# Performance work log

Measured on AMD Instinct MI355X. Metric: run time of the kernel, lower is better.

Reference implementation:

```python
import jax, jax.numpy as jnp
import numpy as np

N_NODES = 100000
N_EDGES = 3200000
F_IN = 128
F_HID = 16
F_OUT = 1


def setup_inputs() -> dict:
    key = jax.random.key(0)
    ks = jax.random.split(key, 8)
    x = jax.random.normal(ks[0], (N_NODES, F_IN), dtype=jnp.float32)
    src = jax.random.randint(ks[1], (N_EDGES,), 0, N_NODES, dtype=jnp.int32)
    dst = jax.random.randint(ks[2], (N_EDGES,), 0, N_NODES, dtype=jnp.int32)
    edge_w = jax.random.uniform(ks[3], (N_EDGES,), dtype=jnp.float32)
    W0 = jax.random.normal(ks[4], (F_IN, F_HID), dtype=jnp.float32) / np.sqrt(F_IN)
    b0 = jnp.zeros((F_HID,), dtype=jnp.float32)
    W1 = jax.random.normal(ks[5], (F_HID, F_OUT), dtype=jnp.float32) / np.sqrt(F_HID)
    b1 = jnp.zeros((F_OUT,), dtype=jnp.float32)
    return {"x": x, "src": src, "dst": dst, "edge_w": edge_w,
            "W0": W0, "b0": b0, "W1": W1, "b1": b1}


def _spmm(src, dst, edge_w, h):
    # sparse A (COO) @ dense h: gather rows at src, weight, scatter-add to dst
    msgs = h[src] * edge_w[:, None]            # [E, F]
    return jax.ops.segment_sum(msgs, dst, num_segments=N_NODES)  # [N, F]


def reference(x, src, dst, edge_w, W0, b0, W1, b1):
    # GCNConv layer 0: relu(A @ (x @ W0) + b0)
    z0 = x @ W0                                 # [N, 16] linear transform first
    h = jax.nn.relu(_spmm(src, dst, edge_w, z0) + b0)
    # (Dropout is identity at inference)
    # GCNConv layer 1: sigmoid(A @ (h @ W1) + b1)
    z1 = h @ W1                                 # [N, 1]
    out = jax.nn.sigmoid(_spmm(src, dst, edge_w, z1) + b1)
    return out
```

## Files before the change

### kernel.cpp

```cpp
#include <hip/hip_runtime.h>

#define N_NODES 100000
#define N_EDGES 3200000
#define F_IN 128
#define F_HID 16

#define BK_LG 7
#define BK_NODES 128
#define NB ((N_NODES + BK_NODES - 1) / BK_NODES)
#define BCAPF 4736
#define CLG 10
#define CNODES 1024
#define NBC ((N_NODES + CNODES - 1) / CNODES)
#define NBC_P 128
#define BCAPC 34816
#define CHUNK1 2048
#define NCH1 ((N_EDGES + CHUNK1 - 1) / CHUNK1)
#define CHUNKM 2048
#define CPB2 ((BCAPC + CHUNKM - 1) / CHUNKM)
#define NMB (NBC * CPB2)
#define NXB ((N_NODES + 63) / 64)
#define PAIRED (2 * NXB)
#define GRID_MID (NMB + NXB)
#define CUR_STRIDE 16

__device__ __forceinline__ unsigned short f2bf_rne(float f) {
    unsigned u = __float_as_uint(f);
    u += 0x7FFFu + ((u >> 16) & 1u);
    return (unsigned short)(u >> 16);
}

__global__ __launch_bounds__(256) void k_bin1(const int* __restrict__ src,
                                              const int* __restrict__ dst,
                                              const float* __restrict__ ew,
                                              int* __restrict__ cursorC,
                                              int2* __restrict__ ebinC) {
    __shared__ int2 stage[CHUNK1];
    __shared__ unsigned char sbid[CHUNK1];
    __shared__ int cnt[NBC_P], excl[NBC_P], run[NBC_P], gb[NBC_P], alw[NBC_P];
    __shared__ int wtot[2];
    const int tid = threadIdx.x;
    const int e0  = blockIdx.x * CHUNK1;
    const int nch = min(CHUNK1, N_EDGES - e0);

    for (int i = tid; i < NBC_P; i += 256) cnt[i] = 0;
    __syncthreads();

    int es[8], eb[8], edl[8]; float ww[8];
    #pragma unroll
    for (int k = 0; k < 8; ++k) {
        int idx = k * 256 + tid;
        if (idx < nch) {
            int e = e0 + idx;
            int d = dst[e];
            es[k]  = src[e];
            ww[k]  = ew[e];
            eb[k]  = d >> CLG;
            edl[k] = d & (CNODES - 1);
            atomicAdd(&cnt[eb[k]], 1);
        } else {
            eb[k] = -1;
        }
    }
    __syncthreads();

    {
        const int lane = tid & 63;
        int inc = 0, dv_ = 0;
        if (tid < NBC_P) {
            dv_ = cnt[tid];
            inc = dv_;
            #pragma unroll
            for (int off = 1; off < 64; off <<= 1) {
                int t = __shfl_up(inc, off);
                if (lane >= off) inc += t;
            }
            if (lane == 63) wtot[tid >> 6] = inc;
        }
        __syncthreads();
        if (tid < NBC_P) {
            int base = (tid >= 64) ? wtot[0] : 0;
            excl[tid] = base + inc - dv_;
        }
    }
    __syncthreads();

    if (tid < NBC) {
        int c = cnt[tid];
        if (c > 0) {
            int old = atomicAdd(&cursorC[tid * CUR_STRIDE], c);
            int a = BCAPC - old;
            a = (a < 0) ? 0 : ((a > c) ? c : a);
            alw[tid] = a;
            gb[tid]  = tid * BCAPC + old;
        } else {
            alw[tid] = 0;
            gb[tid]  = tid * BCAPC;
        }
        run[tid] = 0;
    }
    __syncthreads();

    #pragma unroll
    for (int k = 0; k < 8; ++k) {
        if (eb[k] >= 0) {
            int b = eb[k];
            int p = excl[b] + atomicAdd(&run[b], 1);
            stage[p] = make_int2(__float_as_int(ww[k]), es[k] | (edl[k] << 17));
            sbid[p]  = (unsigned char)b;
        }
    }
    __syncthreads();

    for (int s = tid; s < nch; s += 256) {
        int b   = sbid[s];
        int off = s - excl[b];
        if (off < alw[b]) ebinC[(size_t)gb[b] + off] = stage[s];
    }
}

__global__ __launch_bounds__(256) void k_mid(const int* __restrict__ cursorC,
                                             const int2* __restrict__ ebinC,
                                             int* __restrict__ cursorF,
                                             int2* __restrict__ ebinF,
                                             int* __restrict__ deg,
                                             const float* __restrict__ x,
                                             const float* __restrict__ W0,
                                             unsigned short* __restrict__ z0b) {
    __shared__ __align__(16) char smem[24832];
    const int tid = threadIdx.x;
    const int bid = blockIdx.x;
    int rid; bool isBin;
    if (bid < PAIRED) { isBin = (bid & 1) == 0; rid = bid >> 1; }
    else              { isBin = true; rid = NXB + (bid - PAIRED); }

    if (!isBin) {
        unsigned short* xsb = (unsigned short*)smem;
        float* w0s = (float*)(smem + 16640);
        for (int i = tid; i < F_IN * F_HID; i += 256) w0s[i] = W0[i];
        const int row0 = rid * 64;
        for (int i = tid; i < 64 * 32; i += 256) {
            int r = i >> 5, c4 = i & 31;
            float4 v = make_float4(0.f, 0.f, 0.f, 0.f);
            int row = row0 + r;
            if (row < N_NODES) v = ((const float4*)(x + (size_t)row * F_IN))[c4];
            *(ushort2*)(xsb + r * 130 + c4 * 4)     = make_ushort2(f2bf_rne(v.x), f2bf_rne(v.y));
            *(ushort2*)(xsb + r * 130 + c4 * 4 + 2) = make_ushort2(f2bf_rne(v.z), f2bf_rne(v.w));
        }
        __syncthreads();
        const int r  = tid & 63;
        const int cg = tid >> 6;
        float a0 = 0.f, a1 = 0.f, a2 = 0.f, a3 = 0.f;
        #pragma unroll 4
        for (int k = 0; k < F_IN; k += 2) {
            unsigned u = *(const unsigned*)(xsb + r * 130 + k);
            float xv0 = __uint_as_float(u << 16);
            float xv1 = __uint_as_float(u & 0xFFFF0000u);
            const float* wr0 = w0s + k * F_HID + cg * 4;
            const float* wr1 = wr0 + F_HID;
            a0 = fmaf(xv0, wr0[0], a0); a1 = fmaf(xv0, wr0[1], a1);
            a2 = fmaf(xv0, wr0[2], a2); a3 = fmaf(xv0, wr0[3], a3);
            a0 = fmaf(xv1, wr1[0], a0); a1 = fmaf(xv1, wr1[1], a1);
            a2 = fmaf(xv1, wr1[2], a2); a3 = fmaf(xv1, wr1[3], a3);
        }
        int row = row0 + r;
        if (row < N_NODES) {
            ushort4 p = make_ushort4(f2bf_rne(a0), f2bf_rne(a1),
                                     f2bf_rne(a2), f2bf_rne(a3));
            *(ushort4*)(z0b + (size_t)row * F_HID + cg * 4) = p;
        }
    } else {
        int2* stage = (int2*)smem;
        unsigned char* sbid = (unsigned char*)(smem + 16384);
        int* dcnt   = (int*)(smem + 18432);
        int* cntw   = (int*)(smem + 22528);
        int* runw   = (int*)(smem + 22656);
        int* base   = (int*)(smem + 22784);
        int* totals = (int*)(smem + 23040);
        int* excl_s = (int*)(smem + 23072);
        int* gb8    = (int*)(smem + 23104);
        int* alw8   = (int*)(smem + 23136);
        const int wid = tid >> 6;
        const int c   = rid / CPB2;
        const int ck  = rid % CPB2;
        const int ecnt = min(cursorC[c * CUR_STRIDE], BCAPC);
        const int beg  = ck * CHUNKM;
        const int n2   = min(CHUNKM, ecnt - beg);
        if (n2 <= 0) return;
        const int2* eC = ebinC + (size_t)c * BCAPC + beg;

        if (tid < 32) { cntw[tid] = 0; runw[tid] = 0; }
        for (int i = tid; i < CNODES; i += 256) dcnt[i] = 0;
        __syncthreads();

        int fid[8]; int2 pk[8];
        #pragma unroll
        for (int k = 0; k < 8; ++k) {
            int idx = k * 256 + tid;
            if (idx < n2) {
                int2 e = eC[idx];
                int dlc = e.y >> 17;
                int f   = dlc >> BK_LG;
                fid[k]  = f;
                pk[k]   = make_int2(e.x, (e.y & 0x1FFFF) | ((dlc & (BK_NODES - 1)) << 17));
                atomicAdd(&cntw[f * 4 + wid], 1);
                atomicAdd(&dcnt[dlc], 1);
            } else {
                fid[k] = -1;
            }
        }
        __syncthreads();

        if (tid < 8) {
            int t = 0;
            #pragma unroll
            for (int w = 0; w < 4; ++w) t += cntw[tid * 4 + w];
            totals[tid] = t;
        }
        __syncthreads();
        if (tid < 8) {
            int e = 0;
            for (int f = 0; f < 8; ++f) if (f < tid) e += totals[f];
            excl_s[tid] = e;
            int t = totals[tid];
            int fb = c * 8 + tid;
            if (t > 0 && fb < NB) {
                int old = atomicAdd(&cursorF[fb * CUR_STRIDE], t);
                int a = BCAPF - old;
                a = (a < 0) ? 0 : ((a > t) ? t : a);
                alw8[tid] = a;
                gb8[tid]  = fb * BCAPF + old;
            } else {
                alw8[tid] = 0;
                gb8[tid]  = 0;
            }
        }
        __syncthreads();
        if (tid < 32) {
            int f = tid >> 2, w = tid & 3;
            int bb = excl_s[f];
            for (int w2 = 0; w2 < 4; ++w2) if (w2 < w) bb += cntw[f * 4 + w2];
            base[tid] = bb;
        }
        __syncthreads();

        #pragma unroll
        for (int k = 0; k < 8; ++k) {
            if (fid[k] >= 0) {
                int slot = fid[k] * 4 + wid;
                int p = base[slot] + atomicAdd(&runw[slot], 1);
                stage[p] = pk[k];
                sbid[p]  = (unsigned char)fid[k];
            }
        }
        __syncthreads();

        for (int s = tid; s < n2; s += 256) {
            int f   = sbid[s];
            int off = s - excl_s[f];
            if (off < alw8[f]) ebinF[(size_t)gb8[f] + off] = stage[s];
        }

        for (int i = tid; i < CNODES; i += 256) {
            int d = dcnt[i];
            int v = c * CNODES + i;
            if (d > 0 && v < N_NODES) atomicAdd(&deg[v], d);
        }
    }
}

__global__ __launch_bounds__(512) void k_sg0(const int* __restrict__ deg,
                                             const int2* __restrict__ ebinF,
                                             const unsigned short* __restrict__ z0b,
                                             const float* __restrict__ b0,
                                             const float* __restrict__ W1,
                                             float* __restrict__ z1) {
    __shared__ int2 sorted[BCAPF];
    __shared__ int scn[BK_NODES], dg[BK_NODES], run[BK_NODES];
    __shared__ int wtot[2], ecnt_s;
    __shared__ float b0s[16], w1s[16];
    const int tid  = threadIdx.x;
    const int lane = tid & 63, wid = tid >> 6;
    const int b    = blockIdx.x;
    if (tid < 16) { b0s[tid] = b0[tid]; w1s[tid] = W1[tid]; }

    int inc = 0, d_ = 0;
    if (tid < BK_NODES) {
        int v = b * BK_NODES + tid;
        d_ = (v < N_NODES) ? deg[v] : 0;
        dg[tid]  = d_;
        run[tid] = 0;
        inc = d_;
        #pragma unroll
        for (int off = 1; off < 64; off <<= 1) {
            int t = __shfl_up(inc, off);
            if (lane >= off) inc += t;
        }
        if (lane == 63) wtot[tid >> 6] = inc;
    }
    __syncthreads();
    if (tid < BK_NODES) {
        int base = (tid >= 64) ? wtot[0] : 0;
        scn[tid] = base + inc - d_;
        if (tid == BK_NODES - 1) ecnt_s = min(base + inc, BCAPF);
    }
    __syncthreads();

    const int ecnt = ecnt_s;
    const int2* eb = ebinF + (size_t)b * BCAPF;
    for (int i = tid; i < ecnt; i += 512) {
        int2 e  = eb[i];
        int  dl = e.y >> 17;
        int  p  = scn[dl] + atomicAdd(&run[dl], 1);
        if (p < BCAPF) sorted[p] = e;
    }
    __syncthreads();

    for (int n = wid; n < BK_NODES; n += 8) {
        const int v = b * BK_NODES + n;
        if (v >= N_NODES) continue;
        const int beg = scn[n];
        const int end = min(beg + dg[n], BCAPF);
        const int dv  = end - beg;
        const int f2  = lane & 7;
        const int g   = lane >> 3;
        float acc0 = 0.f, acc1 = 0.f;
        for (int j = g; j < dv; j += 16) {
            int2 e0 = sorted[beg + j];
            int  j1 = j + 8;
            int2 e1 = (j1 < dv) ? sorted[beg + j1] : make_int2(0, 0);
            unsigned u0 = *(const unsigned*)(z0b + (size_t)(e0.y & 0x1FFFF) * F_HID + f2 * 2);
            unsigned u1 = *(const unsigned*)(z0b + (size_t)(e1.y & 0x1FFFF) * F_HID + f2 * 2);
            float w0 = __int_as_float(e0.x), w1 = __int_as_float(e1.x);
            acc0 = fmaf(__uint_as_float(u0 << 16),         w0, acc0);
            acc1 = fmaf(__uint_as_float(u0 & 0xFFFF0000u), w0, acc1);
            acc0 = fmaf(__uint_as_float(u1 << 16),         w1, acc0);
            acc1 = fmaf(__uint_as_float(u1 & 0xFFFF0000u), w1, acc1);
        }
        acc0 += __shfl_xor(acc0, 8);  acc1 += __shfl_xor(acc1, 8);
        acc0 += __shfl_xor(acc0, 16); acc1 += __shfl_xor(acc1, 16);
        acc0 += __shfl_xor(acc0, 32); acc1 += __shfl_xor(acc1, 32);
        float cc = fmaxf(acc0 + b0s[f2 * 2], 0.f) * w1s[f2 * 2]
                 + fmaxf(acc1 + b0s[f2 * 2 + 1], 0.f) * w1s[f2 * 2 + 1];
        cc += __shfl_xor(cc, 1);
        cc += __shfl_xor(cc, 2);
        cc += __shfl_xor(cc, 4);
        if (lane == 0) z1[v] = cc;
    }
}

__global__ __launch_bounds__(256) void k_g1(const int* __restrict__ cursorF,
                                            const int2* __restrict__ ebinF,
                                            const float* __restrict__ z1,
                                            const float* __restrict__ b1,
                                            float* __restrict__ out) {
    __shared__ float acc[BK_NODES];
    const int tid = threadIdx.x;
    const int b   = blockIdx.x;
    if (tid < BK_NODES) acc[tid] = 0.f;
    __syncthreads();
    const int   ecnt = min(cursorF[b * CUR_STRIDE], BCAPF);
    const int2* eb   = ebinF + (size_t)b * BCAPF;
    for (int i = tid; i < ecnt; i += 512) {
        int2 e0 = eb[i];
        int  i1 = i + 256;
        int2 e1 = (i1 < ecnt) ? eb[i1] : make_int2(0, 0);
        float m0 = z1[e0.y & 0x1FFFF] * __int_as_float(e0.x);
        float m1 = z1[e1.y & 0x1FFFF] * __int_as_float(e1.x);
        atomicAdd(&acc[e0.y >> 17], m0);
        if (i1 < ecnt) atomicAdd(&acc[e1.y >> 17], m1);
    }
    __syncthreads();
    if (tid < BK_NODES) {
        int v = b * BK_NODES + tid;
        if (v < N_NODES) out[v] = 1.f / (1.f + expf(-(acc[tid] + b1[0])));
    }
}

extern "C" void kernel_launch(void* const* d_in, const int* in_sizes, int n_in,
                              void* d_out, int out_size, void* d_ws, size_t ws_size,
                              hipStream_t stream) {
    const float* x   = (const float*)d_in[0];
    const int*   src = (const int*)d_in[1];
    const int*   dst = (const int*)d_in[2];
    const float* ew  = (const float*)d_in[3];
    const float* W0  = (const float*)d_in[4];
    const float* b0  = (const float*)d_in[5];
    const float* W1  = (const float*)d_in[6];
    const float* b1  = (const float*)d_in[7];
    float* out = (float*)d_out;

    unsigned short* z0b = (unsigned short*)d_ws;
    float* z1      = (float*)(z0b + (size_t)N_NODES * F_HID);
    int*   deg     = (int*)(z1 + N_NODES);
    int*   cursorC = deg + N_NODES;
    int*   cursorF = cursorC + NBC * CUR_STRIDE;
    int2*  ebinC   = (int2*)(cursorF + NB * CUR_STRIDE);
    int2*  ebinF   = ebinC + (size_t)NBC * BCAPC;

    hipMemsetAsync(deg, 0,
                   ((size_t)N_NODES + (size_t)(NBC + NB) * CUR_STRIDE) * sizeof(int),
                   stream);

    k_bin1<<<NCH1, 256, 0, stream>>>(src, dst, ew, cursorC, ebinC);
    k_mid <<<GRID_MID, 256, 0, stream>>>(cursorC, ebinC, cursorF, ebinF, deg,
                                         x, W0, z0b);
    k_sg0 <<<NB, 512, 0, stream>>>(deg, ebinF, z0b, b0, W1, z1);
    k_g1  <<<NB, 256, 0, stream>>>(cursorF, ebinF, z1, b1, out);
}
```

Measured before the change: 137.6 us.

## Double binning chunk size and use per-wave shared counters in k_bin1

```diff
diff --git a/kernel.cpp b/kernel.cpp
--- a/kernel.cpp
+++ b/kernel.cpp
@@ -14,7 +14,7 @@
 #define NBC ((N_NODES + CNODES - 1) / CNODES)
 #define NBC_P 128
 #define BCAPC 34816
-#define CHUNK1 2048
+#define CHUNK1 4096
 #define NCH1 ((N_EDGES + CHUNK1 - 1) / CHUNK1)
 #define CHUNKM 2048
 #define CPB2 ((BCAPC + CHUNKM - 1) / CHUNKM)
@@ -30,26 +30,30 @@
     return (unsigned short)(u >> 16);
 }
 
-__global__ __launch_bounds__(256) void k_bin1(const int* __restrict__ src,
+__global__ __launch_bounds__(512) void k_bin1(const int* __restrict__ src,
                                               const int* __restrict__ dst,
                                               const float* __restrict__ ew,
                                               int* __restrict__ cursorC,
                                               int2* __restrict__ ebinC) {
     __shared__ int2 stage[CHUNK1];
     __shared__ unsigned char sbid[CHUNK1];
-    __shared__ int cnt[NBC_P], excl[NBC_P], run[NBC_P], gb[NBC_P], alw[NBC_P];
+    __shared__ int cntw[NBC_P * 8];
+    __shared__ int runw[NBC_P * 8];
+    __shared__ int basew[NBC_P * 8];
+    __shared__ int cnt[NBC_P], excl[NBC_P], gb[NBC_P], alw[NBC_P];
     __shared__ int wtot[2];
-    const int tid = threadIdx.x;
-    const int e0  = blockIdx.x * CHUNK1;
-    const int nch = min(CHUNK1, N_EDGES - e0);
-
-    for (int i = tid; i < NBC_P; i += 256) cnt[i] = 0;
+    const int tid  = threadIdx.x;
+    const int lane = tid & 63, wid = tid >> 6;
+    const int e0   = blockIdx.x * CHUNK1;
+    const int nch  = min(CHUNK1, N_EDGES - e0);
+
+    for (int i = tid; i < NBC_P * 8; i += 512) { cntw[i] = 0; runw[i] = 0; }
     __syncthreads();
 
     int es[8], eb[8], edl[8]; float ww[8];
     #pragma unroll
     for (int k = 0; k < 8; ++k) {
-        int idx = k * 256 + tid;
+        int idx = k * 512 + tid;
         if (idx < nch) {
             int e = e0 + idx;
             int d = dst[e];
@@ -57,34 +61,37 @@
             ww[k]  = ew[e];
             eb[k]  = d >> CLG;
             edl[k] = d & (CNODES - 1);
-            atomicAdd(&cnt[eb[k]], 1);
+            atomicAdd(&cntw[eb[k] * 8 + wid], 1);
         } else {
             eb[k] = -1;
         }
     }
     __syncthreads();
 
-    {
-        const int lane = tid & 63;
-        int inc = 0, dv_ = 0;
-        if (tid < NBC_P) {
-            dv_ = cnt[tid];
-            inc = dv_;
-            #pragma unroll
-            for (int off = 1; off < 64; off <<= 1) {
-                int t = __shfl_up(inc, off);
-                if (lane >= off) inc += t;
-            }
-            if (lane == 63) wtot[tid >> 6] = inc;
-        }
-        __syncthreads();
-        if (tid < NBC_P) {
-            int base = (tid >= 64) ? wtot[0] : 0;
-            excl[tid] = base + inc - dv_;
-        }
-    }
-    __syncthreads();
-
+    if (tid < NBC_P) {
+        int t = 0;
+        #pragma unroll
+        for (int w = 0; w < 8; ++w) t += cntw[tid * 8 + w];
+        cnt[tid] = t;
+    }
+    __syncthreads();
+
+    int inc = 0, c_ = 0;
+    if (tid < NBC_P) {
+        c_ = cnt[tid];
+        inc = c_;
+        #pragma unroll
+        for (int off = 1; off < 64; off <<= 1) {
+            int t = __shfl_up(inc, off);
+            if (lane >= off) inc += t;
+        }
+        if (lane == 63) wtot[tid >> 6] = inc;
+    }
+    __syncthreads();
+    if (tid < NBC_P) {
+        int base = (tid >= 64) ? wtot[0] : 0;
+        excl[tid] = base + inc - c_;
+    }
     if (tid < NBC) {
         int c = cnt[tid];
         if (c > 0) {
@@ -97,7 +104,13 @@
             alw[tid] = 0;
             gb[tid]  = tid * BCAPC;
         }
-        run[tid] = 0;
+    }
+    __syncthreads();
+
+    if (tid < NBC_P) {
+        int bb = excl[tid];
+        #pragma unroll
+        for (int w = 0; w < 8; ++w) { basew[tid * 8 + w] = bb; bb += cntw[tid * 8 + w]; }
     }
     __syncthreads();
 
@@ -105,14 +118,14 @@
     for (int k = 0; k < 8; ++k) {
         if (eb[k] >= 0) {
             int b = eb[k];
-            int p = excl[b] + atomicAdd(&run[b], 1);
+            int p = basew[b * 8 + wid] + atomicAdd(&runw[b * 8 + wid], 1);
             stage[p] = make_int2(__float_as_int(ww[k]), es[k] | (edl[k] << 17));
             sbid[p]  = (unsigned char)b;
         }
     }
     __syncthreads();
 
-    for (int s = tid; s < nch; s += 256) {
+    for (int s = tid; s < nch; s += 512) {
         int b   = sbid[s];
         int off = s - excl[b];
         if (off < alw[b]) ebinC[(size_t)gb[b] + off] = stage[s];
@@ -402,7 +415,7 @@
                    ((size_t)N_NODES + (size_t)(NBC + NB) * CUR_STRIDE) * sizeof(int),
                    stream);
 
-    k_bin1<<<NCH1, 256, 0, stream>>>(src, dst, ew, cursorC, ebinC);
+    k_bin1<<<NCH1, 512, 0, stream>>>(src, dst, ew, cursorC, ebinC);
     k_mid <<<GRID_MID, 256, 0, stream>>>(cursorC, ebinC, cursorF, ebinF, deg,
                                          x, W0, z0b);
     k_sg0 <<<NB, 512, 0, stream>>>(deg, ebinF, z0b, b0, W1, z1);
```

Measured after the change: 125.6 us. 1.1x faster.
